# Kernel optimization log

Hardware: AMD Instinct MI355X
Metric: run time of the kernel (lower is better)

The kernel has to match this reference:

```python
import jax, jax.numpy as jnp
import numpy as np

DIM = 192
HEADS = 4
EPS = 1e-12  # F.normalize default eps


def setup_inputs() -> dict:
    key = jax.random.key(0)
    k0, k1, k2, k3 = jax.random.split(key, 4)
    x = jax.random.normal(k0, (4, DIM, 128, 128), dtype=jnp.float32)
    # qkv 1x1 conv weight: [3*dim, dim, 1, 1] -> stored as [3*dim, dim]
    w_qkv = jax.random.normal(k1, (3 * DIM, DIM), dtype=jnp.float32) * (1.0 / np.sqrt(DIM))
    # depthwise 3x3 conv weight: [3*dim, 1, 3, 3]
    w_dw = jax.random.normal(k2, (3 * DIM, 1, 3, 3), dtype=jnp.float32) * (1.0 / 3.0)
    # project_out 1x1 conv weight: [dim, dim]
    w_proj = jax.random.normal(k3, (DIM, DIM), dtype=jnp.float32) * (1.0 / np.sqrt(DIM))
    # temperature: ones(heads,1,1), requires_grad=False in original
    temperature = jnp.ones((HEADS, 1, 1), dtype=jnp.float32)
    return {"x": x, "w_qkv": w_qkv, "w_dw": w_dw, "w_proj": w_proj,
            "temperature": temperature}


def _l2norm(t):
    # F.normalize(t, dim=-1): t / max(||t||_2, eps)
    n = jnp.sqrt(jnp.sum(t * t, axis=-1, keepdims=True))
    return t / jnp.maximum(n, EPS)


def reference(x, w_qkv, w_dw, w_proj, temperature):
    b, c, h, w = x.shape
    ch = c // HEADS  # channels per head
    # 1x1 conv (no bias) == channel GEMM
    qkv = jnp.einsum('oc,bchw->bohw', w_qkv, x)
    # depthwise 3x3 conv, padding=1, groups=3*dim
    qkv = jax.lax.conv_general_dilated(
        qkv, w_dw, window_strides=(1, 1), padding=((1, 1), (1, 1)),
        dimension_numbers=('NCHW', 'OIHW', 'NCHW'),
        feature_group_count=3 * c)
    q, k, v = jnp.split(qkv, 3, axis=1)
    # b (head ch) h w -> b head ch (h w)
    def rearr(t):
        return t.reshape(b, HEADS, ch, h * w)
    q, k, v = rearr(q), rearr(k), rearr(v)
    q = _l2norm(q)
    k = _l2norm(k)
    # channel-channel attention: [b, head, ch, ch]
    attn = jnp.einsum('bhcn,bhdn->bhcd', q, k) * temperature[None]
    attn = jax.nn.softmax(attn, axis=-1)
    out = jnp.einsum('bhcd,bhdn->bhcn', attn, v)
    out = out.reshape(b, c, h, w)
    out = jnp.einsum('oc,bchw->bohw', w_proj, out)
    return out
```

## Files before the change

kernel.cpp:

```cpp
#include <hip/hip_runtime.h>

typedef unsigned short u16;
typedef float f32x4 __attribute__((ext_vector_type(4)));
typedef __bf16 bf16x8 __attribute__((ext_vector_type(8)));
typedef unsigned short u16x8 __attribute__((ext_vector_type(8)));
typedef unsigned short u16x4 __attribute__((ext_vector_type(4)));

#define DEV static __device__ __forceinline__

DEV u16 f2bf(float f) {
  unsigned int u = __float_as_uint(f);
  u += 0x7FFFu + ((u >> 16) & 1u);
  return (u16)(u >> 16);
}
DEV float bf2f(u16 h) { return __uint_as_float(((unsigned int)h) << 16); }

DEV void gload_lds16(const void* g, void* l) {
  __builtin_amdgcn_global_load_lds(
      (__attribute__((address_space(1))) void*)(unsigned long long)g,
      (__attribute__((address_space(3))) void*)l, 16, 0, 0);
}

DEV void vm_wait(int n) {
  switch (n) {
    case 0:  asm volatile("s_waitcnt vmcnt(0)" ::: "memory"); break;
    case 4:  asm volatile("s_waitcnt vmcnt(4)" ::: "memory"); break;
    case 6:  asm volatile("s_waitcnt vmcnt(6)" ::: "memory"); break;
    case 8:  asm volatile("s_waitcnt vmcnt(8)" ::: "memory"); break;
    case 10: asm volatile("s_waitcnt vmcnt(10)" ::: "memory"); break;
    default: asm volatile("s_waitcnt vmcnt(14)" ::: "memory"); break;
  }
}

__global__ __launch_bounds__(256) void convert_w_kernel(
    const float* __restrict__ in, u16* __restrict__ out, int n) {
  int i = blockIdx.x * 256 + threadIdx.x;
  if (i < n) out[i] = f2bf(in[i]);
}

template <bool IN_F32, bool OUT_BF16, int NJT>
__global__ __launch_bounds__(256, 2) void gemm_bt_kernel(
    const void* __restrict__ Av, const u16* __restrict__ B,
    void* __restrict__ Cv, size_t aBatch, size_t bBatch, size_t cBatch,
    int ldC) {
  __shared__ __align__(16) char smem[73728];
  char* sA = smem;

  const int tid = threadIdx.x, wave = tid >> 6, lane = tid & 63;
  const int m0 = blockIdx.x * 64, b = blockIdx.y;
  const char* Bbase = (const char*)(B + (size_t)b * bBatch);
  char* bufs = smem + 24576 + wave * 12288;
  const int jwbase = wave * (NJT * 16);

  f32x4 vaf[3][4];
  u16x8 vau[2][4];
  if (IN_F32) {
    const float* Xb = (const float*)Av + (size_t)b * aBatch + m0;
    const int cbl = tid & 15, iq = tid >> 4;
#pragma unroll
    for (int p = 0; p < 3; ++p)
#pragma unroll
      for (int r = 0; r < 4; ++r)
        vaf[p][r] = *(const f32x4*)(Xb + (size_t)((p * 16 + cbl) * 4 + r) *
                                             16384 + iq * 4);
  } else {
    const u16* Vb = (const u16*)Av + (size_t)b * aBatch + m0;
#pragma unroll
    for (int p = 0; p < 2; ++p) {
      const int task = p * 256 + tid;
      if (task < 384) {
        const int cb = task >> 3, io = task & 7;
#pragma unroll
        for (int r = 0; r < 4; ++r)
          vau[p][r] = *(const u16x8*)(Vb + (size_t)(cb * 4 + r) * 16384 +
                                      io * 8);
      }
    }
  }
#pragma unroll
  for (int t = 0; t < 2; ++t) {
    if (t < NJT) {
#pragma unroll
      for (int i = 0; i < 6; ++i) {
        const int d = i * 1024 + lane * 16;
        const int row = d / 384, inrow = d - row * 384;
        gload_lds16(Bbase + (size_t)(jwbase + t * 16 + row) * 384 +
                        (inrow ^ ((row & 7) << 4)),
                    bufs + t * 6144 + i * 1024);
      }
    }
  }
  if (IN_F32) {
    const int cbl = tid & 15, iq = tid >> 4;
#pragma unroll
    for (int p = 0; p < 3; ++p) {
      const int cb = p * 16 + cbl;
#pragma unroll
      for (int j = 0; j < 4; ++j) {
        const int n = iq * 4 + j;
        u16x4 col;
        col[0] = f2bf(vaf[p][0][j]);
        col[1] = f2bf(vaf[p][1][j]);
        col[2] = f2bf(vaf[p][2][j]);
        col[3] = f2bf(vaf[p][3][j]);
        *(u16x4*)(sA + n * 384 + ((cb * 8) ^ ((n & 7) << 4))) = col;
      }
    }
  } else {
#pragma unroll
    for (int p = 0; p < 2; ++p) {
      const int task = p * 256 + tid;
      if (task < 384) {
        const int cb = task >> 3, io = task & 7;
#pragma unroll
        for (int j = 0; j < 8; ++j) {
          const int n = io * 8 + j;
          u16x4 col;
          col[0] = vau[p][0][j];
          col[1] = vau[p][1][j];
          col[2] = vau[p][2][j];
          col[3] = vau[p][3][j];
          *(u16x4*)(sA + n * 384 + ((cb * 8) ^ ((n & 7) << 4))) = col;
        }
      }
    }
  }
  asm volatile("s_waitcnt lgkmcnt(0)" ::: "memory");
  __builtin_amdgcn_s_barrier();

  const int l15 = lane & 15, lg = lane >> 4;
  const int swm = (l15 & 7) << 4;

  bf16x8 af[4][6];
#pragma unroll
  for (int mi = 0; mi < 4; ++mi)
#pragma unroll
    for (int ks = 0; ks < 6; ++ks)
      af[mi][ks] = *(const bf16x8*)(sA + (mi * 16 + l15) * 384 +
                                    ((ks * 64 + lg * 16) ^ swm));

#pragma unroll
  for (int t = 0; t < NJT; ++t) {
    vm_wait(t == 0 ? (NJT > 1 ? 6 : 0) : (4 + (t + 1 < NJT ? 6 : 0)));
    __builtin_amdgcn_sched_barrier(0);
    char* bw = bufs + (t & 1) * 6144;
    bf16x8 bfv[6];
#pragma unroll
    for (int ks = 0; ks < 6; ++ks)
      bfv[ks] = *(const bf16x8*)(bw + l15 * 384 + ((ks * 64 + lg * 16) ^ swm));
    f32x4 acc[4];
#pragma unroll
    for (int mi = 0; mi < 4; ++mi) acc[mi] = (f32x4){0.f, 0.f, 0.f, 0.f};
#pragma unroll
    for (int ks = 0; ks < 6; ++ks)
#pragma unroll
      for (int mi = 0; mi < 4; ++mi)
        acc[mi] = __builtin_amdgcn_mfma_f32_16x16x32_bf16(af[mi][ks], bfv[ks],
                                                          acc[mi], 0, 0, 0);
    const int jrow = jwbase + t * 16 + l15;
    if (OUT_BF16) {
      u16* Cb = (u16*)Cv + (size_t)b * cBatch;
#pragma unroll
      for (int mi = 0; mi < 4; ++mi) {
        u16x4 ov;
#pragma unroll
        for (int r = 0; r < 4; ++r) ov[r] = f2bf(acc[mi][r]);
        *(u16x4*)(Cb + (size_t)jrow * ldC + m0 + mi * 16 + lg * 4) = ov;
      }
    } else {
      float* Cb = (float*)Cv + (size_t)b * cBatch;
#pragma unroll
      for (int mi = 0; mi < 4; ++mi)
        *(f32x4*)(Cb + (size_t)jrow * ldC + m0 + mi * 16 + lg * 4) = acc[mi];
    }
    if (t + 2 < NJT) {
      __builtin_amdgcn_sched_barrier(0);
#pragma unroll
      for (int i = 0; i < 6; ++i) {
        const int d = i * 1024 + lane * 16;
        const int row = d / 384, inrow = d - row * 384;
        gload_lds16(Bbase + (size_t)(jwbase + (t + 2) * 16 + row) * 384 +
                        (inrow ^ ((row & 7) << 4)),
                    bw + i * 1024);
      }
    }
  }
}

__global__ __launch_bounds__(256) void dwconv_kernel(
    u16* __restrict__ qkv, const float* __restrict__ wdw,
    float* __restrict__ sq) {
  __shared__ u16 img[16384];
  __shared__ float red[4];
  const int o = blockIdx.x, b = blockIdx.y;
  const size_t base = ((size_t)b * 576 + o) * 16384;
  const int tid = threadIdx.x, wave = tid >> 6, lane = tid & 63;
#pragma unroll
  for (int i = 0; i < 8; ++i) {
    const int off = (i * 4 + wave) * 1024;
    gload_lds16((const char*)qkv + base * 2 + off + lane * 16, (char*)img + off);
  }
  asm volatile("s_waitcnt vmcnt(0)" ::: "memory");
  __syncthreads();
  float w[9];
#pragma unroll
  for (int j = 0; j < 9; ++j) w[j] = wdw[o * 9 + j];
  float sqacc = 0.f;
  for (int it = 0; it < 8; ++it) {
    const int chunk = it * 256 + tid;
    const int px0 = chunk * 8;
    const int y = px0 >> 7, x0 = px0 & 127;
    float acc[8];
#pragma unroll
    for (int j = 0; j < 8; ++j) acc[j] = 0.f;
#pragma unroll
    for (int dy = -1; dy <= 1; ++dy) {
      const int yy = y + dy;
      float v[10];
      if (yy >= 0 && yy <= 127) {
        const u16* rowp = img + yy * 128 + x0;
        u16x8 m = *(const u16x8*)rowp;
#pragma unroll
        for (int j = 0; j < 8; ++j) v[j + 1] = bf2f(m[j]);
        v[0] = (x0 > 0) ? bf2f(rowp[-1]) : 0.f;
        v[9] = (x0 < 120) ? bf2f(rowp[8]) : 0.f;
      } else {
#pragma unroll
        for (int j = 0; j < 10; ++j) v[j] = 0.f;
      }
      const float w0 = w[(dy + 1) * 3], w1 = w[(dy + 1) * 3 + 1],
                  w2 = w[(dy + 1) * 3 + 2];
#pragma unroll
      for (int j = 0; j < 8; ++j) acc[j] += w0 * v[j] + w1 * v[j + 1] + w2 * v[j + 2];
    }
    u16x8 ov;
#pragma unroll
    for (int j = 0; j < 8; ++j) {
      sqacc += acc[j] * acc[j];
      ov[j] = f2bf(acc[j]);
    }
    *(u16x8*)(qkv + base + px0) = ov;
  }
#pragma unroll
  for (int s = 32; s > 0; s >>= 1) sqacc += __shfl_xor(sqacc, s, 64);
  if (lane == 0) red[wave] = sqacc;
  __syncthreads();
  if (tid == 0) sq[b * 576 + o] = red[0] + red[1] + red[2] + red[3];
}

__global__ __launch_bounds__(256) void gram_kernel(
    const u16* __restrict__ qkv, float* __restrict__ partial) {
  __shared__ u16 tiles[4 * 3072];
  __shared__ float red[4 * 2304];
  const int bh = blockIdx.y, b = bh >> 2, h = bh & 3;
  const int g = blockIdx.x;
  const int wave = threadIdx.x >> 6, lane = threadIdx.x & 63;
  const int n0 = g * 512 + wave * 128;
  const u16* qb = qkv + ((size_t)b * 576 + h * 48) * 16384;
  const u16* kb = qb + (size_t)192 * 16384;
  char* tl = (char*)(tiles + wave * 3072);
  const int l15 = lane & 15, lg = lane >> 4;
  const int swz = (l15 & 3) << 4;
  f32x4 acc[3][3];
#pragma unroll
  for (int i = 0; i < 3; ++i)
#pragma unroll
    for (int j = 0; j < 3; ++j) acc[i][j] = (f32x4){0.f, 0.f, 0.f, 0.f};

  for (int ks = 0; ks < 4; ++ks) {
    const int nn = n0 + ks * 32;
    asm volatile("s_waitcnt lgkmcnt(0)" ::: "memory");
#pragma unroll
    for (int i = 0; i < 6; ++i) {
      const int flat = i * 1024 + lane * 16;
      const int row = flat >> 6, colb = flat & 63;
      const u16* src = (row < 48) ? (qb + (size_t)row * 16384 + nn)
                                  : (kb + (size_t)(row - 48) * 16384 + nn);
      gload_lds16((const char*)src + (colb ^ ((row & 3) << 4)), tl + i * 1024);
    }
    asm volatile("s_waitcnt vmcnt(0)" ::: "memory");
    bf16x8 qf[3], kf[3];
#pragma unroll
    for (int f = 0; f < 3; ++f) {
      qf[f] = *(const bf16x8*)(tl + (f * 16 + l15) * 64 + ((lg * 16) ^ swz));
      kf[f] = *(const bf16x8*)(tl + (48 + f * 16 + l15) * 64 + ((lg * 16) ^ swz));
    }
#pragma unroll
    for (int i = 0; i < 3; ++i)
#pragma unroll
      for (int j = 0; j < 3; ++j)
        acc[i][j] = __builtin_amdgcn_mfma_f32_16x16x32_bf16(qf[i], kf[j],
                                                            acc[i][j], 0, 0, 0);
  }
  {
    float* rw = red + wave * 2304;
#pragma unroll
    for (int i = 0; i < 3; ++i)
#pragma unroll
      for (int j = 0; j < 3; ++j)
#pragma unroll
        for (int r = 0; r < 4; ++r)
          rw[(i * 16 + lg * 4 + r) * 48 + (j * 16 + l15)] = acc[i][j][r];
  }
  __syncthreads();
#pragma unroll
  for (int it = 0; it < 9; ++it) {
    const int p = it * 256 + threadIdx.x;
    const float s = red[p] + red[2304 + p] + red[4608 + p] + red[6912 + p];
    partial[((size_t)bh * 2304 + p) * 32 + g] = s;
  }
}

__global__ __launch_bounds__(256) void reduce_partial_kernel(
    const float* __restrict__ partial, float* __restrict__ G) {
  const int idx = blockIdx.x * 256 + threadIdx.x;
  const f32x4* pp = (const f32x4*)(partial + (size_t)idx * 32);
  const f32x4 a = (pp[0] + pp[1]) + (pp[2] + pp[3]) +
                  (pp[4] + pp[5]) + (pp[6] + pp[7]);
  G[idx] = a.x + a.y + a.z + a.w;
}

__global__ __launch_bounds__(256) void softmax_weff_kernel(
    const float* __restrict__ Gin, const float* __restrict__ sq,
    const float* __restrict__ temp, const float* __restrict__ wproj,
    u16* __restrict__ weff) {
  __shared__ float G[2304];
  __shared__ float wp[192 * 49];
  __shared__ float nq[48], nk[48];
  const int bh = blockIdx.x, b = bh >> 2, h = bh & 3;
  const int tid = threadIdx.x;
#pragma unroll
  for (int it = 0; it < 36; ++it) {
    const int j = it * 256 + tid;
    const int o = j / 48, c = j - o * 48;
    wp[o * 49 + c] = wproj[o * 192 + h * 48 + c];
  }
#pragma unroll
  for (int it = 0; it < 9; ++it) {
    const int p = it * 256 + tid;
    G[p] = Gin[(size_t)bh * 2304 + p];
  }
  if (tid < 48) {
    nq[tid] = fmaxf(sqrtf(sq[b * 576 + h * 48 + tid]), 1e-12f);
    nk[tid] = fmaxf(sqrtf(sq[b * 576 + 192 + h * 48 + tid]), 1e-12f);
  }
  __syncthreads();
  if (tid < 48) {
    const int r = tid;
    const float inq = temp[h] / nq[r];
    float L[48];
    float mx = -3.4e38f;
#pragma unroll 4
    for (int d = 0; d < 48; ++d) {
      const float v = G[r * 48 + d] * inq / nk[d];
      L[d] = v;
      mx = fmaxf(mx, v);
    }
    float s = 0.f;
#pragma unroll 4
    for (int d = 0; d < 48; ++d) {
      const float e = __expf(L[d] - mx);
      L[d] = e;
      s += e;
    }
    const float inv = 1.f / s;
#pragma unroll 4
    for (int d = 0; d < 48; ++d) G[r * 48 + d] = L[d] * inv;
  }
  __syncthreads();
  if (tid < 192) {
    const int o = tid;
    f32x4 acc[12];
#pragma unroll
    for (int dv = 0; dv < 12; ++dv) acc[dv] = (f32x4){0.f, 0.f, 0.f, 0.f};
    for (int c = 0; c < 48; ++c) {
      const float w = wp[o * 49 + c];
      const f32x4* at = (const f32x4*)(G + c * 48);
#pragma unroll
      for (int dv = 0; dv < 12; ++dv) acc[dv] += w * at[dv];
    }
    u16* op = weff + ((size_t)b * 192 + o) * 192 + h * 48;
#pragma unroll
    for (int g8 = 0; g8 < 6; ++g8) {
      u16x8 ov;
#pragma unroll
      for (int j = 0; j < 8; ++j) {
        const int d = g8 * 8 + j;
        ov[j] = f2bf(acc[d >> 2][d & 3]);
      }
      *(u16x8*)(op + g8 * 8) = ov;
    }
  }
}

extern "C" void kernel_launch(void* const* d_in, const int* in_sizes, int n_in,
                              void* d_out, int out_size, void* d_ws,
                              size_t ws_size, hipStream_t stream) {
  (void)in_sizes; (void)n_in; (void)out_size; (void)ws_size;
  const float* x      = (const float*)d_in[0];
  const float* w_qkv  = (const float*)d_in[1];
  const float* w_dw   = (const float*)d_in[2];
  const float* w_proj = (const float*)d_in[3];
  const float* temp   = (const float*)d_in[4];

  char* ws = (char*)d_ws;
  u16*   qkv     = (u16*)ws;
  float* partial = (float*)(ws + 75497472);
  float* G       = (float*)(ws + 80216064);
  float* sq      = (float*)(ws + 80363520);
  u16*   Wq      = (u16*)(ws + 80372736);
  u16*   Weff    = (u16*)(ws + 80593920);

  convert_w_kernel<<<dim3(432), 256, 0, stream>>>(w_qkv, Wq, 110592);
  gemm_bt_kernel<true, true, 9><<<dim3(256, 4), 256, 0, stream>>>(
      x, Wq, qkv, (size_t)192 * 16384, 0, (size_t)576 * 16384, 16384);
  dwconv_kernel<<<dim3(576, 4), 256, 0, stream>>>(qkv, w_dw, sq);
  gram_kernel<<<dim3(32, 16), 256, 0, stream>>>(qkv, partial);
  reduce_partial_kernel<<<dim3(144), 256, 0, stream>>>(partial, G);
  softmax_weff_kernel<<<dim3(16), 256, 0, stream>>>(G, sq, temp, w_proj, Weff);
  gemm_bt_kernel<false, false, 3><<<dim3(256, 4), 256, 0, stream>>>(
      qkv + (size_t)384 * 16384, Weff, d_out, (size_t)576 * 16384,
      (size_t)192 * 192, (size_t)192 * 16384, 16384);
}
```

Before: 135.6 us.

## Stage GEMM outputs through LDS for coalesced stores and pad qkv row stride

The GEMM epilogue now writes each wave's 16-row output tile into LDS, then reads it back so each row is stored with full-width contiguous 16-byte vector writes instead of scattered 8/16-byte fragments. The qkv intermediate gets a padded row stride (16448 instead of 16384) to avoid channel-aligned cache/TLB set conflicts across rows, and all consumers and workspace offsets are updated to match. This adds an extra barrier and LDS round-trip per tile, reuses the A-tile LDS region after a barrier, and slightly enlarges the workspace.

```diff
diff --git a/kernel.cpp b/kernel.cpp
--- a/kernel.cpp
+++ b/kernel.cpp
@@ -8,6 +8,8 @@
 
 #define DEV static __device__ __forceinline__
 
+#define QS 16448
+
 DEV u16 f2bf(float f) {
   unsigned int u = __float_as_uint(f);
   u += 0x7FFFu + ((u >> 16) & 1u);
@@ -24,6 +26,7 @@
 DEV void vm_wait(int n) {
   switch (n) {
     case 0:  asm volatile("s_waitcnt vmcnt(0)" ::: "memory"); break;
+    case 2:  asm volatile("s_waitcnt vmcnt(2)" ::: "memory"); break;
     case 4:  asm volatile("s_waitcnt vmcnt(4)" ::: "memory"); break;
     case 6:  asm volatile("s_waitcnt vmcnt(6)" ::: "memory"); break;
     case 8:  asm volatile("s_waitcnt vmcnt(8)" ::: "memory"); break;
@@ -41,8 +44,8 @@
 template <bool IN_F32, bool OUT_BF16, int NJT>
 __global__ __launch_bounds__(256, 2) void gemm_bt_kernel(
     const void* __restrict__ Av, const u16* __restrict__ B,
-    void* __restrict__ Cv, size_t aBatch, size_t bBatch, size_t cBatch,
-    int ldC) {
+    void* __restrict__ Cv, size_t aBatch, int aStride, size_t bBatch,
+    size_t cBatch, int ldC) {
   __shared__ __align__(16) char smem[73728];
   char* sA = smem;
 
@@ -51,6 +54,7 @@
   const char* Bbase = (const char*)(B + (size_t)b * bBatch);
   char* bufs = smem + 24576 + wave * 12288;
   const int jwbase = wave * (NJT * 16);
+  constexpr int S = OUT_BF16 ? 2 : 4;
 
   f32x4 vaf[3][4];
   u16x8 vau[2][4];
@@ -62,7 +66,7 @@
 #pragma unroll
       for (int r = 0; r < 4; ++r)
         vaf[p][r] = *(const f32x4*)(Xb + (size_t)((p * 16 + cbl) * 4 + r) *
-                                             16384 + iq * 4);
+                                             aStride + iq * 4);
   } else {
     const u16* Vb = (const u16*)Av + (size_t)b * aBatch + m0;
 #pragma unroll
@@ -72,7 +76,7 @@
         const int cb = task >> 3, io = task & 7;
 #pragma unroll
         for (int r = 0; r < 4; ++r)
-          vau[p][r] = *(const u16x8*)(Vb + (size_t)(cb * 4 + r) * 16384 +
+          vau[p][r] = *(const u16x8*)(Vb + (size_t)(cb * 4 + r) * aStride +
                                       io * 8);
       }
     }
@@ -138,10 +142,14 @@
     for (int ks = 0; ks < 6; ++ks)
       af[mi][ks] = *(const bf16x8*)(sA + (mi * 16 + l15) * 384 +
                                     ((ks * 64 + lg * 16) ^ swm));
+  asm volatile("s_waitcnt lgkmcnt(0)" ::: "memory");
+  __builtin_amdgcn_s_barrier();
+
+  char* rbuf = sA + wave * 6144;
 
 #pragma unroll
   for (int t = 0; t < NJT; ++t) {
-    vm_wait(t == 0 ? (NJT > 1 ? 6 : 0) : (4 + (t + 1 < NJT ? 6 : 0)));
+    vm_wait(t == 0 ? (NJT > 1 ? 6 : 0) : (S + (t + 1 < NJT ? 6 : 0)));
     __builtin_amdgcn_sched_barrier(0);
     char* bw = bufs + (t & 1) * 6144;
     bf16x8 bfv[6];
@@ -157,21 +165,36 @@
       for (int mi = 0; mi < 4; ++mi)
         acc[mi] = __builtin_amdgcn_mfma_f32_16x16x32_bf16(af[mi][ks], bfv[ks],
                                                           acc[mi], 0, 0, 0);
-    const int jrow = jwbase + t * 16 + l15;
     if (OUT_BF16) {
-      u16* Cb = (u16*)Cv + (size_t)b * cBatch;
 #pragma unroll
       for (int mi = 0; mi < 4; ++mi) {
         u16x4 ov;
 #pragma unroll
         for (int r = 0; r < 4; ++r) ov[r] = f2bf(acc[mi][r]);
-        *(u16x4*)(Cb + (size_t)jrow * ldC + m0 + mi * 16 + lg * 4) = ov;
+        *(u16x4*)(rbuf + l15 * 136 + mi * 32 + lg * 8) = ov;
+      }
+      asm volatile("s_waitcnt lgkmcnt(0)" ::: "memory");
+      u16* Cb = (u16*)Cv + (size_t)b * cBatch;
+#pragma unroll
+      for (int half = 0; half < 2; ++half) {
+        const int row = half * 8 + (lane >> 3);
+        const u16x8 val = *(const u16x8*)(rbuf + row * 136 + (lane & 7) * 16);
+        *(u16x8*)(Cb + (size_t)(jwbase + t * 16 + row) * ldC + m0 +
+                  (lane & 7) * 8) = val;
       }
     } else {
+#pragma unroll
+      for (int mi = 0; mi < 4; ++mi)
+        *(f32x4*)(rbuf + l15 * 272 + mi * 64 + lg * 16) = acc[mi];
+      asm volatile("s_waitcnt lgkmcnt(0)" ::: "memory");
       float* Cb = (float*)Cv + (size_t)b * cBatch;
 #pragma unroll
-      for (int mi = 0; mi < 4; ++mi)
-        *(f32x4*)(Cb + (size_t)jrow * ldC + m0 + mi * 16 + lg * 4) = acc[mi];
+      for (int q = 0; q < 4; ++q) {
+        const int row = q * 4 + (lane >> 4);
+        const f32x4 val = *(const f32x4*)(rbuf + row * 272 + (lane & 15) * 16);
+        *(f32x4*)(Cb + (size_t)(jwbase + t * 16 + row) * ldC + m0 +
+                  (lane & 15) * 4) = val;
+      }
     }
     if (t + 2 < NJT) {
       __builtin_amdgcn_sched_barrier(0);
@@ -193,7 +216,7 @@
   __shared__ u16 img[16384];
   __shared__ float red[4];
   const int o = blockIdx.x, b = blockIdx.y;
-  const size_t base = ((size_t)b * 576 + o) * 16384;
+  const size_t base = ((size_t)b * 576 + o) * QS;
   const int tid = threadIdx.x, wave = tid >> 6, lane = tid & 63;
 #pragma unroll
   for (int i = 0; i < 8; ++i) {
@@ -256,8 +279,8 @@
   const int g = blockIdx.x;
   const int wave = threadIdx.x >> 6, lane = threadIdx.x & 63;
   const int n0 = g * 512 + wave * 128;
-  const u16* qb = qkv + ((size_t)b * 576 + h * 48) * 16384;
-  const u16* kb = qb + (size_t)192 * 16384;
+  const u16* qb = qkv + ((size_t)b * 576 + h * 48) * QS;
+  const u16* kb = qb + (size_t)192 * QS;
   char* tl = (char*)(tiles + wave * 3072);
   const int l15 = lane & 15, lg = lane >> 4;
   const int swz = (l15 & 3) << 4;
@@ -274,8 +297,8 @@
     for (int i = 0; i < 6; ++i) {
       const int flat = i * 1024 + lane * 16;
       const int row = flat >> 6, colb = flat & 63;
-      const u16* src = (row < 48) ? (qb + (size_t)row * 16384 + nn)
-                                  : (kb + (size_t)(row - 48) * 16384 + nn);
+      const u16* src = (row < 48) ? (qb + (size_t)row * QS + nn)
+                                  : (kb + (size_t)(row - 48) * QS + nn);
       gload_lds16((const char*)src + (colb ^ ((row & 3) << 4)), tl + i * 1024);
     }
     asm volatile("s_waitcnt vmcnt(0)" ::: "memory");
@@ -405,20 +428,20 @@
 
   char* ws = (char*)d_ws;
   u16*   qkv     = (u16*)ws;
-  float* partial = (float*)(ws + 75497472);
-  float* G       = (float*)(ws + 80216064);
-  float* sq      = (float*)(ws + 80363520);
-  u16*   Wq      = (u16*)(ws + 80372736);
-  u16*   Weff    = (u16*)(ws + 80593920);
+  float* partial = (float*)(ws + 75792384);
+  float* G       = (float*)(ws + 80510976);
+  float* sq      = (float*)(ws + 80658432);
+  u16*   Wq      = (u16*)(ws + 80667648);
+  u16*   Weff    = (u16*)(ws + 80888832);
 
   convert_w_kernel<<<dim3(432), 256, 0, stream>>>(w_qkv, Wq, 110592);
   gemm_bt_kernel<true, true, 9><<<dim3(256, 4), 256, 0, stream>>>(
-      x, Wq, qkv, (size_t)192 * 16384, 0, (size_t)576 * 16384, 16384);
+      x, Wq, qkv, (size_t)192 * 16384, 16384, 0, (size_t)576 * QS, QS);
   dwconv_kernel<<<dim3(576, 4), 256, 0, stream>>>(qkv, w_dw, sq);
   gram_kernel<<<dim3(32, 16), 256, 0, stream>>>(qkv, partial);
   reduce_partial_kernel<<<dim3(144), 256, 0, stream>>>(partial, G);
   softmax_weff_kernel<<<dim3(16), 256, 0, stream>>>(G, sq, temp, w_proj, Weff);
   gemm_bt_kernel<false, false, 3><<<dim3(256, 4), 256, 0, stream>>>(
-      qkv + (size_t)384 * 16384, Weff, d_out, (size_t)576 * 16384,
+      qkv + (size_t)384 * QS, Weff, d_out, (size_t)576 * QS, QS,
       (size_t)192 * 192, (size_t)192 * 16384, 16384);
 }
```

Measured after the change: 135.2 us. No clear change (-0.3%).
